# Optimization experiments

Measured on AMD Instinct MI355X. Metric: run time of the kernel, lower is better.

## Reference

```python
import jax, jax.numpy as jnp
import numpy as np
from jax.scipy.special import logsumexp

G, H, L, N, K = 2000, 128, 10, 4096, 10
TAU, LC, LA, EPS = 0.1, 1.0, 0.5, 1e-6

def _lin_init(k, fi, fo):
    return jax.random.normal(k, (fi, fo), jnp.float32) / np.sqrt(fi)

def setup_inputs():
    key = jax.random.key(0)
    ks = jax.random.split(key, 12)
    return {
        'wt_x': jax.random.normal(ks[0], (N, G), jnp.float32),
        'ko_x': jax.random.normal(ks[1], (N, G), jnp.float32),
        'wt_labels': jax.random.randint(ks[2], (N,), 0, K, dtype=jnp.int32),
        'ko_labels': jax.random.randint(ks[3], (N,), 0, K, dtype=jnp.int32),
        'enc_w1': _lin_init(ks[4], G, H), 'enc_b1': jnp.zeros((H,)),
        'enc_g': jnp.ones((H,)), 'enc_be': jnp.zeros((H,)),
        'enc_w2': _lin_init(ks[5], H, L), 'enc_b2': jnp.zeros((L,)),
        'kap_w1': _lin_init(ks[6], G, H), 'kap_b1': jnp.zeros((H,)),
        'kap_g': jnp.ones((H,)), 'kap_be': jnp.zeros((H,)),
        'kap_w2': _lin_init(ks[7], H, 1), 'kap_b2': jnp.zeros((1,)),
        'dec_w1': _lin_init(ks[8], L, H), 'dec_b1': jnp.zeros((H,)),
        'dec_g': jnp.ones((H,)), 'dec_be': jnp.zeros((H,)),
        'dec_w2': _lin_init(ks[9], H, G), 'dec_b2': jnp.zeros((G,)),
    }

def _mlp(x, w1, b1, g, be, w2, b2):
    # Linear -> LayerNorm -> ReLU -> Linear (dropout_prob=0)
    h = x @ w1 + b1
    m = h.mean(-1, keepdims=True)
    v = ((h - m) ** 2).mean(-1, keepdims=True)
    h = (h - m) / jnp.sqrt(v + 1e-5) * g + be
    return jax.nn.relu(h) @ w2 + b2

def _contrastive(z_wt, z_ko, y_wt, y_ko):
    S = (z_wt @ z_ko.T) / TAU  # [Nwt, Nko], unit-norm z so |S| <= 1/tau
    total = jnp.float32(0.0)
    n_shared = jnp.float32(0.0)
    for c in range(K):  # fixed small class count
        mwt = (y_wt == c).astype(S.dtype)
        mko = (y_ko == c).astype(S.dtype)
        n_wt, n_ko = mwt.sum(), mko.sum()
        valid = (n_wt > 0) & (n_ko > 0)
        nw, nk = jnp.maximum(n_wt, 1.0), jnp.maximum(n_ko, 1.0)
        # mean_{i in c, j in c} (LSE_i - S_ij) over ko columns of class c
        lse_r = logsumexp(jnp.where(mko[None, :] > 0, S, -1e4), axis=1)
        l1 = jnp.sum(mwt * (lse_r - (S @ mko) / nk)) / nw
        lse_c = logsumexp(jnp.where(mwt[:, None] > 0, S, -1e4), axis=0)
        l2 = jnp.sum(mko * (lse_c - (mwt @ S) / nw)) / nk
        total = total + jnp.where(valid, 0.5 * (l1 + l2), 0.0)
        n_shared = n_shared + valid.astype(S.dtype)
    return jnp.where(n_shared > 0, total / jnp.maximum(n_shared, 1.0), 0.0)

def _alignment(z, y):
    ones = jnp.ones(z.shape[0], z.dtype)
    counts = jax.ops.segment_sum(ones, y, num_segments=K)
    mu_c = jax.ops.segment_sum(z, y, num_segments=K) / jnp.maximum(counts, 1.0)[:, None]
    dev = z - mu_c[y]
    per_class = jax.ops.segment_sum(jnp.sum(dev ** 2, axis=1), y, num_segments=K) / jnp.maximum(counts, 1.0)
    present = counts > 0
    return jnp.sum(jnp.where(present, per_class, 0.0)) / jnp.maximum(jnp.sum(present.astype(z.dtype)), 1.0)

def reference(wt_x, ko_x, enc_w1, enc_b1, enc_g, enc_be, enc_w2, enc_b2, kap_w1, kap_b1, kap_g, kap_be, kap_w2, kap_b2, dec_w1, dec_b1, dec_g, dec_be, dec_w2, dec_b2, wt_labels, ko_labels):
    def encode(x):
        mu = _mlp(x, enc_w1, enc_b1, enc_g, enc_be, enc_w2, enc_b2)
        mu = mu / jnp.maximum(jnp.linalg.norm(mu, axis=1, keepdims=True), 1e-12)
        kappa = jax.nn.softplus(_mlp(x, kap_w1, kap_b1, kap_g, kap_be, kap_w2, kap_b2)) + EPS
        return mu, kappa
    wt_mu, wt_kappa = encode(wt_x)
    ko_mu, ko_kappa = encode(ko_x)
    wt_z, ko_z = wt_mu, ko_mu  # eval mode: z = mu (deterministic)
    wt_rec = _mlp(wt_z, dec_w1, dec_b1, dec_g, dec_be, dec_w2, dec_b2)
    ko_rec = _mlp(ko_z, dec_w1, dec_b1, dec_g, dec_be, dec_w2, dec_b2)
    recon = jnp.mean((wt_rec - wt_x) ** 2) + jnp.mean((ko_rec - ko_x) ** 2)
    kl = (wt_kappa.mean() + ko_kappa.mean()) * 0.01
    contrast = _contrastive(wt_z, ko_z, wt_labels, ko_labels)
    align = _alignment(jnp.concatenate([wt_z, ko_z], 0), jnp.concatenate([wt_labels, ko_labels], 0))
    return recon + kl + LC * contrast + LA * align
```

## Files before the change

kernel.cpp:

```cpp
#include <hip/hip_runtime.h>
#include <math.h>

typedef __attribute__((ext_vector_type(8))) __bf16 bf16x8;
typedef __attribute__((ext_vector_type(4))) float f32x4;

#define GL2LDS_(gptr, lptr) \
    __builtin_amdgcn_global_load_lds((const __attribute__((address_space(1))) void*)(gptr), \
                                     (__attribute__((address_space(3))) void*)(lptr), 16, 0, 0)

#define OFF_NWT   0
#define OFF_NKO   10
#define OFF_L1    20
#define OFF_L2    30
#define OFF_CNT   40
#define OFF_ZSUM  50
#define OFF_ZSQ   150
#define OFF_KSUM  160
#define OFF_REC   162
#define IOFF_WTOFF 192
#define IOFF_KOOFF 204
#define IOFF_WTCTR 216
#define IOFF_KOCTR 226
#define ACC_FLOATS 256

// ... 58 lines not shown
    for (int i = 0; i < 32; ++i) {
        int idx = i * 256 + t;
        int c = idx >> 6, jj = idx & 63;
        int j = j0 + jj;
        tile[jj][c] = (j < 2000) ? dw2[(size_t)c * 2000 + j] : 0.f;
    }
    __syncthreads();
#pragma unroll
    for (int i = 0; i < 32; ++i) {
        int idx = i * 256 + t;
        int jj = idx >> 7, c = idx & 127;
        float v = tile[jj][c];
        __bf16 h = (__bf16)v;
        size_t o = (size_t)(j0 + jj) * 128 + c;
        BThi[o] = h;
        BTlo[o] = (__bf16)(v - (float)h);
    }
}

__global__ void counts_kernel(const int* __restrict__ wtl, const int* __restrict__ kol,
                              float* __restrict__ acc)
{
    __shared__ int cw[10], ck[10];
    int t = threadIdx.x;
    if (t < 10) { cw[t] = 0; ck[t] = 0; }
    __syncthreads();
    for (int i = t; i < 4096; i += 1024) {
        atomicAdd(&cw[wtl[i]], 1);
        atomicAdd(&ck[kol[i]], 1);
    }
    __syncthreads();
    if (t < 10) { acc[OFF_NWT + t] = (float)cw[t]; acc[OFF_NKO + t] = (float)ck[t]; }
    if (t == 0) {
        int* ai = (int*)acc;
        int aw = 0, ak = 0;
        for (int c = 0; c < 10; ++c) {
            ai[IOFF_WTOFF + c] = aw; aw += cw[c];
            ai[IOFF_KOOFF + c] = ak; ak += ck[c];
        }
        ai[IOFF_WTOFF + 10] = aw;
        ai[IOFF_KOOFF + 10] = ak;
    }
}

__global__ __launch_bounds__(256) void scatter_z_kernel(const float* __restrict__ Z,
                                                        const int* __restrict__ wtl,
                                                        const int* __restrict__ kol,
                                                        float* __restrict__ acc,
                                                        float* __restrict__ ZcWT,
                                                        float* __restrict__ ZcKO)
{
    __shared__ int lcnt[20];
    __shared__ int lbase[20];
    int t = threadIdx.x;
    if (t < 20) lcnt[t] = 0;
    __syncthreads();
    int row = blockIdx.x * 256 + t;
    int side = row >= 4096;
    int r = side ? row - 4096 : row;
    int c = side ? kol[r] : wtl[r];
    int key = side * 10 + c;
    int myrank = atomicAdd(&lcnt[key], 1);
    __syncthreads();
    int* ai = (int*)acc;
    if (t < 20 && lcnt[t] > 0)
        lbase[t] = atomicAdd(&ai[IOFF_WTCTR + t], lcnt[t]);
    __syncthreads();
    int off = side ? ai[IOFF_KOOFF + c] : ai[IOFF_WTOFF + c];
    int slot = off + lbase[key] + myrank;
    float* dst = side ? ZcKO : ZcWT;
    const float* zr = Z + (size_t)row * 10;
#pragma unroll
    for (int d = 0; d < 10; ++d) dst[d * 4096 + slot] = zr[d];
}

__global__ __launch_bounds__(512) void gemm1_kernel(const float* __restrict__ wt_x,
                                                    const float* __restrict__ ko_x,
                                                    const __bf16* __restrict__ WThi,
                                                    const __bf16* __restrict__ WTlo,
                                                    float* __restrict__ Hb,
                                                    float* __restrict__ Hrest,
                                                    int nkc)
{
    __shared__ short Bs[2][2][4096];
    int t = threadIdx.x;
    int widx = t >> 6, lane = t & 63;
    int wm = widx >> 1, wn = widx & 1;
    int b = blockIdx.x;
    int mt = b & 63, strip = (b >> 6) & 1, kc = b >> 7;
    int R0 = mt * 128;
    int cb = strip * 128;
    int kchunk = 2048 / nkc;
    int kbase = kc * kchunk;
    int kleft = 2000 - kbase;
    int nsteps = (kleft < kchunk) ? ((kleft + 31) >> 5) : (kchunk >> 5);

    const float* xb = (R0 < 4096) ? (wt_x + (size_t)R0 * 2000)
                                  : (ko_x + (size_t)(R0 - 4096) * 2000);
    int ar = wm * 32 + (lane & 15);
    const float* xrow0 = xb + (size_t)ar * 2000 + kbase;
    const float* xrow1 = xrow0 + (size_t)16 * 2000;
    int kboff = (lane >> 4) * 8;

    int col0 = t >> 2;
    int s0   = (t & 3) ^ ((col0 >> 1) & 3);
    size_t boff = (size_t)(cb + col0) * 2048 + kbase + s0 * 8;
    const __bf16* bsrcH = WThi + boff;
    const __bf16* bsrcL = WTlo + boff;
    short* dstH0 = &Bs[0][0][t * 8];
    short* dstL0 = &Bs[0][1][t * 8];
    short* dstH1 = &Bs[1][0][t * 8];
    short* dstL1 = &Bs[1][1][t * 8];

    f32x4 acc00, acc01, acc02, acc03;
    f32x4 acc10, acc11, acc12, acc13;
#pragma unroll
    for (int r = 0; r < 4; ++r) {
        acc00[r]=0.f; acc01[r]=0.f; acc02[r]=0.f; acc03[r]=0.f;
        acc10[r]=0.f; acc11[r]=0.f; acc12[r]=0.f; acc13[r]=0.f;
    }

    float4 aA00, aA01, aA10, aA11;
    float4 aB00, aB01, aB10, aB11;

#define GLOADA_(step, a00, a01, a10, a11) do { \
    int k0_ = (step) * 32; \
    int k_ = k0_ + kboff; \
    if (kbase + k0_ <= 1952) { \
        a00 = *(const float4*)(xrow0 + k_); \
        a01 = *(const float4*)(xrow0 + k_ + 4); \
        a10 = *(const float4*)(xrow1 + k_); \
        a11 = *(const float4*)(xrow1 + k_ + 4); \
    } else { \
        float t0_[8], t1_[8]; \
        _Pragma("unroll") \
        for (int j = 0; j < 8; ++j) { \
            int kk = kbase + k_ + j; \
            t0_[j] = (kk < 2000) ? xrow0[k_ + j] : 0.f; \
            t1_[j] = (kk < 2000) ? xrow1[k_ + j] : 0.f; } \
        a00 = make_float4(t0_[0], t0_[1], t0_[2], t0_[3]); \
        a01 = make_float4(t0_[4], t0_[5], t0_[6], t0_[7]); \
        a10 = make_float4(t1_[0], t1_[1], t1_[2], t1_[3]); \
        a11 = make_float4(t1_[4], t1_[5], t1_[6], t1_[7]); } } while (0)

#define CONVA_(a0, a1, ahi, alo) do { \
    float av_[8] = {a0.x, a0.y, a0.z, a0.w, a1.x, a1.y, a1.z, a1.w}; \
    _Pragma("unroll") \
    for (int j = 0; j < 8; ++j) { \
        __bf16 h_ = (__bf16)av_[j]; \
        ahi[j] = h_; \
        alo[j] = (__bf16)(av_[j] - (float)h_); } } while (0)

#define MFMA_(buf, ahi0, alo0, ahi1, alo1) do { \
    _Pragma("unroll") \
    for (int nf = 0; nf < 4; ++nf) { \
        bf16x8 bhf = *(const bf16x8*)&Bs[buf][0][(ubase + nf * 64) * 8]; \
        bf16x8 blf = *(const bf16x8*)&Bs[buf][1][(ubase + nf * 64) * 8]; \
        f32x4* a0 = (nf == 0) ? &acc00 : (nf == 1) ? &acc01 : (nf == 2) ? &acc02 : &acc03; \
        f32x4* a1 = (nf == 0) ? &acc10 : (nf == 1) ? &acc11 : (nf == 2) ? &acc12 : &acc13; \
        *a0 = __builtin_amdgcn_mfma_f32_16x16x32_bf16(ahi0, bhf, *a0, 0, 0, 0); \
        *a0 = __builtin_amdgcn_mfma_f32_16x16x32_bf16(alo0, bhf, *a0, 0, 0, 0); \
        *a0 = __builtin_amdgcn_mfma_f32_16x16x32_bf16(ahi0, blf, *a0, 0, 0, 0); \
        *a1 = __builtin_amdgcn_mfma_f32_16x16x32_bf16(ahi1, bhf, *a1, 0, 0, 0); \
        *a1 = __builtin_amdgcn_mfma_f32_16x16x32_bf16(alo1, bhf, *a1, 0, 0, 0); \
        *a1 = __builtin_amdgcn_mfma_f32_16x16x32_bf16(ahi1, blf, *a1, 0, 0, 0); } } while (0)

    GL2LDS_(bsrcH, dstH0);
    GL2LDS_(bsrcL, dstL0);
    GLOADA_(0, aA00, aA01, aA10, aA11);
    if (1 < nsteps) GLOADA_(1, aB00, aB01, aB10, aB11);
    __syncthreads();

    int cpr = lane & 15;
    int pph = (lane >> 4) ^ ((cpr >> 1) & 3);
    int ubase = (wn * 64 + cpr) * 4 + pph;

    int niter = (nsteps + 1) >> 1;
    for (int it = 0; it < niter; ++it) {
        int st0 = it * 2;
        {
            if (st0 + 1 < nsteps) {
                GL2LDS_(bsrcH + (size_t)(st0 + 1) * 32, dstH1);
                GL2LDS_(bsrcL + (size_t)(st0 + 1) * 32, dstL1);
            }
            bf16x8 ahi0, alo0, ahi1, alo1;
            CONVA_(aA00, aA01, ahi0, alo0);
            CONVA_(aA10, aA11, ahi1, alo1);
            if (st0 + 2 < nsteps) GLOADA_(st0 + 2, aA00, aA01, aA10, aA11);
            MFMA_(0, ahi0, alo0, ahi1, alo1);
            __syncthreads();
        }
        if (st0 + 1 < nsteps) {
            if (st0 + 2 < nsteps) {
                GL2LDS_(bsrcH + (size_t)(st0 + 2) * 32, dstH0);
                GL2LDS_(bsrcL + (size_t)(st0 + 2) * 32, dstL0);
            }
            bf16x8 ahi0, alo0, ahi1, alo1;
            CONVA_(aB00, aB01, ahi0, alo0);
            CONVA_(aB10, aB11, ahi1, alo1);
            if (st0 + 3 < nsteps) GLOADA_(st0 + 3, aB00, aB01, aB10, aB11);
            MFMA_(1, ahi0, alo0, ahi1, alo1);
            __syncthreads();
        }
    }

    float* Hq = (kc == 0) ? Hb : (Hrest + (size_t)(kc - 1) * HPART);
#pragma unroll
    for (int r = 0; r < 4; ++r) {
        int row0 = R0 + wm * 32 + (lane >> 4) * 4 + r;
        size_t base0 = (size_t)row0 * 256 + cb + wn * 64 + (lane & 15);
        Hq[base0]      = acc00[r];
        Hq[base0 + 16] = acc01[r];
        Hq[base0 + 32] = acc02[r];
        Hq[base0 + 48] = acc03[r];
        size_t base1 = base0 + (size_t)16 * 256;
        Hq[base1]      = acc10[r];
        Hq[base1 + 16] = acc11[r];
        Hq[base1 + 32] = acc12[r];
        Hq[base1 + 48] = acc13[r];
    }
#undef GLOADA_
#undef CONVA_
#undef MFMA_
}

__global__ __launch_bounds__(128) void stage2_kernel(const float* __restrict__ Hb,
    const float* __restrict__ Hrest, int nkc,
    const float* __restrict__ enc_b1, const float* __restrict__ enc_g, const float* __restrict__ enc_be,
    const float* __restrict__ enc_w2, const float* __restrict__ enc_b2,
    const float* __restrict__ kap_b1, const float* __restrict__ kap_g, const float* __restrict__ kap_be,
    const float* __restrict__ kap_w2, const float* __restrict__ kap_b2,
    float* __restrict__ Z, float* __restrict__ Kap)
{
    __shared__ float sh[128];
    int row  = blockIdx.x;
    int wave = threadIdx.x >> 6;
    int lane = threadIdx.x & 63;
    size_t hoff = (size_t)row * 256 + wave * 128;
    const float* hb  = Hb + hoff;
    const float* b1 = wave ? kap_b1 : enc_b1;
    const float* gg = wave ? kap_g  : enc_g;
    const float* bb = wave ? kap_be : enc_be;

    float h0 = hb[lane]      + b1[lane];
    float h1 = hb[lane + 64] + b1[lane + 64];
    for (int j = 0; j + 1 < nkc; ++j) {
        const float* hr = Hrest + (size_t)j * HPART + hoff;
        h0 += hr[lane];
        h1 += hr[lane + 64];
    }
    float s = h0 + h1;
#pragma unroll
    for (int o = 32; o > 0; o >>= 1) s += __shfl_xor(s, o, 64);
    float m = s * (1.f / 128.f);
    float d0 = h0 - m, d1 = h1 - m;
    float v = d0 * d0 + d1 * d1;
#pragma unroll
    for (int o = 32; o > 0; o >>= 1) v += __shfl_xor(v, o, 64);
    v *= (1.f / 128.f);
    float sc = 1.f / sqrtf(v + 1e-5f);
    float r0 = fmaxf(fmaf(d0 * sc, gg[lane],      bb[lane]),      0.f);
    float r1 = fmaxf(fmaf(d1 * sc, gg[lane + 64], bb[lane + 64]), 0.f);

    if (wave == 0) { sh[lane] = r0; sh[lane + 64] = r1; }
    __syncthreads();

    if (wave == 0) {
        float mu = 0.f;
        if (lane < 10) {
            mu = enc_b2[lane];
            for (int c = 0; c < 128; ++c) mu = fmaf(sh[c], enc_w2[c * 10 + lane], mu);
        }
        float n2 = mu * mu;
#pragma unroll
        for (int o = 8; o > 0; o >>= 1) n2 += __shfl_xor(n2, o, 16);
        float inv = 1.f / fmaxf(sqrtf(n2), 1e-12f);
        if (lane < 10) Z[(size_t)row * 10 + lane] = mu * inv;
    } else {
        float p = r0 * kap_w2[lane] + r1 * kap_w2[lane + 64];
#pragma unroll
        for (int o = 32; o > 0; o >>= 1) p += __shfl_xor(p, o, 64);
        if (lane == 0) {
            float x = p + kap_b2[0];
            float sp = (x > 20.f) ? x : log1pf(expf(x));
            Kap[row] = sp + 1e-6f;
        }
    }
}

__global__ __launch_bounds__(256) void dec_act_kernel(const float* __restrict__ Zb,
    const float* __restrict__ dw1, const float* __restrict__ db1,
    const float* __restrict__ dg,  const float* __restrict__ dbe,
    __bf16* __restrict__ Ahi, __bf16* __restrict__ Alo)
{
    int wave = threadIdx.x >> 6;
    int lane = threadIdx.x & 63;
    int row = blockIdx.x * 4 + wave;
    const float* zr = Zb + (size_t)row * 10;
    float z[10];
#pragma unroll
    for (int d = 0; d < 10; ++d) z[d] = zr[d];
    int c0 = lane, c1 = lane + 64;
    float h0 = db1[c0], h1 = db1[c1];
#pragma unroll
    for (int d = 0; d < 10; ++d) {
        h0 = fmaf(z[d], dw1[d * 128 + c0], h0);
        h1 = fmaf(z[d], dw1[d * 128 + c1], h1);
    }
    float s = h0 + h1;
#pragma unroll
    for (int o = 32; o > 0; o >>= 1) s += __shfl_xor(s, o, 64);
    float m = s * (1.f / 128.f);
    float d0 = h0 - m, d1 = h1 - m;
    float v = d0 * d0 + d1 * d1;
#pragma unroll
    for (int o = 32; o > 0; o >>= 1) v += __shfl_xor(v, o, 64);
    v *= (1.f / 128.f);
    float sc = 1.f / sqrtf(v + 1e-5f);
    float a0 = fmaxf(fmaf(d0 * sc, dg[c0], dbe[c0]), 0.f);
    float a1 = fmaxf(fmaf(d1 * sc, dg[c1], dbe[c1]), 0.f);
    __bf16 h0b = (__bf16)a0, h1b = (__bf16)a1;
    size_t base = (size_t)row * 128;
    Ahi[base + c0] = h0b;                 Ahi[base + c1] = h1b;
    Alo[base + c0] = (__bf16)(a0 - (float)h0b);
    Alo[base + c1] = (__bf16)(a1 - (float)h1b);
}

__global__ __launch_bounds__(512, 4) void dec_gemm_kernel(
    const __bf16* __restrict__ Ahi, const __bf16* __restrict__ Alo,
    const __bf16* __restrict__ BThi, const __bf16* __restrict__ BTlo,
    const float* __restrict__ wt_x, const float* __restrict__ ko_x,
    const float* __restrict__ db2, float* __restrict__ acc)
{
    __shared__ short BsH[2][8192];
    __shared__ short BsL[2][8192];
    __shared__ float rs[8];
    int t = threadIdx.x;
    int widx = t >> 6, lane = t & 63;
    int wm = widx >> 2, wn = widx & 3;
    int R0 = (blockIdx.x >> 1) * 32;
    int T0 = (blockIdx.x & 1) * 16;
    const float* xbase = (R0 < 4096) ? wt_x : ko_x;
    int xr0 = ((R0 < 4096) ? R0 : R0 - 4096) + wm * 16 + (lane >> 4) * 4;

    size_t abase = (size_t)(R0 + wm * 16 + (lane & 15)) * 128 + (lane >> 4) * 8;
    bf16x8 ah0 = *(const bf16x8*)(Ahi + abase);
    bf16x8 ah1 = *(const bf16x8*)(Ahi + abase + 32);
    bf16x8 ah2 = *(const bf16x8*)(Ahi + abase + 64);
    bf16x8 ah3 = *(const bf16x8*)(Ahi + abase + 96);
    bf16x8 al0 = *(const bf16x8*)(Alo + abase);
    bf16x8 al1 = *(const bf16x8*)(Alo + abase + 32);
    bf16x8 al2 = *(const bf16x8*)(Alo + abase + 64);
    bf16x8 al3 = *(const bf16x8*)(Alo + abase + 96);

    int g0c = t >> 4,         g0s = t & 15;
    int g1c = (t + 512) >> 4, g1s = t & 15;
    int u0 = g0c * 16 + (g0s ^ (g0c & 7));
    int u1 = g1c * 16 + (g1s ^ (g1c & 7));

    int col_local = wn * 16 + (lane & 15);
    int cl7 = col_local & 7;
    int rb = col_local * 16;
    int sb = lane >> 4;

    uint4 hA0, hA1, lA0, lA1, hB0, hB1, lB0, lB1;

#define GLOADB_(tile, h0, h1, l0, l1) do { \
    size_t gb = (size_t)(tile) * 8192; \
    h0 = *(const uint4*)(BThi + gb + (size_t)t * 8); \
    h1 = *(const uint4*)(BThi + gb + (size_t)(t + 512) * 8); \
    l0 = *(const uint4*)(BTlo + gb + (size_t)t * 8); \
    l1 = *(const uint4*)(BTlo + gb + (size_t)(t + 512) * 8); } while (0)

#define DSWRITE_(buf, h0, h1, l0, l1) do { \
    *(uint4*)&BsH[buf][u0 * 8] = h0; \
    *(uint4*)&BsH[buf][u1 * 8] = h1; \
    *(uint4*)&BsL[buf][u0 * 8] = l0; \
    *(uint4*)&BsL[buf][u1 * 8] = l1; } while (0)

#define COMPUTE_(buf, tile) do { \
    int un0 = rb + ((sb +  0) ^ cl7); \
    int un1 = rb + ((sb +  4) ^ cl7); \
    int un2 = rb + ((sb +  8) ^ cl7); \
    int un3 = rb + ((sb + 12) ^ cl7); \
    bf16x8 bh0 = *(const bf16x8*)&BsH[buf][un0 * 8]; \
    bf16x8 bh1 = *(const bf16x8*)&BsH[buf][un1 * 8]; \
    bf16x8 bh2 = *(const bf16x8*)&BsH[buf][un2 * 8]; \
    bf16x8 bh3 = *(const bf16x8*)&BsH[buf][un3 * 8]; \
    bf16x8 bl0 = *(const bf16x8*)&BsL[buf][un0 * 8]; \
    bf16x8 bl1 = *(const bf16x8*)&BsL[buf][un1 * 8]; \
    bf16x8 bl2 = *(const bf16x8*)&BsL[buf][un2 * 8]; \
    bf16x8 bl3 = *(const bf16x8*)&BsL[buf][un3 * 8]; \
    f32x4 a4; \
    _Pragma("unroll") \
    for (int r = 0; r < 4; ++r) a4[r] = 0.f; \
    a4 = __builtin_amdgcn_mfma_f32_16x16x32_bf16(ah0, bh0, a4, 0, 0, 0); \
    a4 = __builtin_amdgcn_mfma_f32_16x16x32_bf16(al0, bh0, a4, 0, 0, 0); \
    a4 = __builtin_amdgcn_mfma_f32_16x16x32_bf16(ah0, bl0, a4, 0, 0, 0); \
    a4 = __builtin_amdgcn_mfma_f32_16x16x32_bf16(ah1, bh1, a4, 0, 0, 0); \
    a4 = __builtin_amdgcn_mfma_f32_16x16x32_bf16(al1, bh1, a4, 0, 0, 0); \
    a4 = __builtin_amdgcn_mfma_f32_16x16x32_bf16(ah1, bl1, a4, 0, 0, 0); \
    a4 = __builtin_amdgcn_mfma_f32_16x16x32_bf16(ah2, bh2, a4, 0, 0, 0); \
    a4 = __builtin_amdgcn_mfma_f32_16x16x32_bf16(al2, bh2, a4, 0, 0, 0); \
    a4 = __builtin_amdgcn_mfma_f32_16x16x32_bf16(ah2, bl2, a4, 0, 0, 0); \
    a4 = __builtin_amdgcn_mfma_f32_16x16x32_bf16(ah3, bh3, a4, 0, 0, 0); \
    a4 = __builtin_amdgcn_mfma_f32_16x16x32_bf16(al3, bh3, a4, 0, 0, 0); \
    a4 = __builtin_amdgcn_mfma_f32_16x16x32_bf16(ah3, bl3, a4, 0, 0, 0); \
    int col = (tile) * 64 + col_local; \
    if (col < 2000) { \
        float bb = db2[col]; \
        _Pragma("unroll") \
        for (int r = 0; r < 4; ++r) { \
            float xv = xbase[(size_t)(xr0 + r) * 2000 + col]; \
            float e = a4[r] + bb - xv; \
            rsum = fmaf(e, e, rsum); \
        } } } while (0)

    float rsum = 0.f;
    GLOADB_(T0 + 0, hA0, hA1, lA0, lA1);
    GLOADB_(T0 + 1, hB0, hB1, lB0, lB1);
    DSWRITE_(0, hA0, hA1, lA0, lA1);
    __syncthreads();

    for (int it = 0; it < 8; ++it) {
        int lt = it * 2;
        {
            if (lt + 2 < 16) GLOADB_(T0 + lt + 2, hA0, hA1, lA0, lA1);
            DSWRITE_(1, hB0, hB1, lB0, lB1);
            COMPUTE_(0, T0 + lt);
            __syncthreads();
        }
        {
            if (lt + 3 < 16) GLOADB_(T0 + lt + 3, hB0, hB1, lB0, lB1);
            if (lt + 2 < 16) DSWRITE_(0, hA0, hA1, lA0, lA1);
            COMPUTE_(1, T0 + lt + 1);
            __syncthreads();
        }
    }

#pragma unroll
    for (int o = 32; o > 0; o >>= 1) rsum += __shfl_xor(rsum, o, 64);
    if (lane == 0) rs[widx] = rsum;
    __syncthreads();
    if (t == 0) {
        float s = 0.f;
#pragma unroll
        for (int w = 0; w < 8; ++w) s += rs[w];
        atomicAdd(&acc[OFF_REC], s);
    }
#undef GLOADB_
#undef DSWRITE_
#undef COMPUTE_
}

#define MAXNB 768
__global__ __launch_bounds__(256) void contrast_kernel(const float* __restrict__ ZcWT,
                                                       const float* __restrict__ ZcKO,
                                                       float* __restrict__ acc)
{
    __shared__ float zb[MAXNB * 12];
    __shared__ float bsum[4];
    int b = blockIdx.x;
    int cs = b / 3, sub = b - cs * 3;
    int c = cs >> 1, side = cs & 1;
    const int* ai = (const int*)acc;
    int aStart = side ? ai[IOFF_KOOFF + c]     : ai[IOFF_WTOFF + c];
    int aEnd   = side ? ai[IOFF_KOOFF + c + 1] : ai[IOFF_WTOFF + c + 1];
    int bStart = side ? ai[IOFF_WTOFF + c]     : ai[IOFF_KOOFF + c];
    int bEnd   = side ? ai[IOFF_WTOFF + c + 1] : ai[IOFF_KOOFF + c + 1];
    int na = aEnd - aStart;
    int nb = bEnd - bStart;
    if (nb > MAXNB) nb = MAXNB;
    const float* ZA = side ? ZcKO : ZcWT;
    const float* ZB = side ? ZcWT : ZcKO;
    int t = threadIdx.x;

    for (int u = t; u < nb; u += 256) {
#pragma unroll
        for (int d = 0; d < 10; ++d) zb[u * 12 + d] = ZB[d * 4096 + bStart + u];
    }
    __syncthreads();

    int chunk = (na + 2) / 3;
    int r0 = sub * chunk;
    int rcnt = na - r0; if (rcnt > chunk) rcnt = chunk;

    float wsum = 0.f;
    bool waveActive = (nb > 0) && ((t & ~63) < rcnt);
    if (waveActive) {
        bool valid = t < rcnt;
        int ar = aStart + (valid ? (r0 + t) : 0);
        float za[10];
#pragma unroll
        for (int d = 0; d < 10; ++d) za[d] = ZA[d * 4096 + ar];
        float se = 0.f, ss = 0.f;
        for (int u = 0; u < nb; ++u) {
            const float* zp = &zb[u * 12];
            float s = 0.f;
#pragma unroll
            for (int d = 0; d < 10; ++d) s = fmaf(za[d], zp[d], s);
            s *= 10.f;
            se += __expf(s - 10.f);
            ss += s;
        }
        if (valid) wsum = (10.f + __logf(se)) - ss / (float)nb;
    }
#pragma unroll
    for (int o = 32; o > 0; o >>= 1) wsum += __shfl_xor(wsum, o, 64);
    if ((t & 63) == 0) bsum[t >> 6] = wsum;
    __syncthreads();
    if (t == 0) {
        float s = bsum[0] + bsum[1] + bsum[2] + bsum[3];
        if (s != 0.f || nb > 0)
            atomicAdd(&acc[(side ? OFF_L2 : OFF_L1) + c], s);
    }
}

__global__ __launch_bounds__(256) void align_kernel(const float* __restrict__ Z,
                                                    const int* __restrict__ wtl,
                                                    const int* __restrict__ kol,
                                                    const float* __restrict__ Kap,
                                                    float* __restrict__ Part)
{
    __shared__ float cL[10], qL[10], sL[100], ks;
    int t = threadIdx.x;
    if (t < 10) { cL[t] = 0.f; qL[t] = 0.f; }
    if (t < 100) sL[t] = 0.f;
    if (t == 0) ks = 0.f;
    __syncthreads();
    int row = blockIdx.x * 256 + t;
    int c = (row < 4096) ? wtl[row] : kol[row - 4096];
    float zz[10]; float q = 0.f;
#pragma unroll
    for (int d = 0; d < 10; ++d) { zz[d] = Z[(size_t)row * 10 + d]; q = fmaf(zz[d], zz[d], q); }
    atomicAdd(&cL[c], 1.f);
    atomicAdd(&qL[c], q);
#pragma unroll
    for (int d = 0; d < 10; ++d) atomicAdd(&sL[c * 10 + d], zz[d]);
    atomicAdd(&ks, Kap[row]);
    __syncthreads();
    float* pb = Part + (size_t)blockIdx.x * 128;
    if (t < 10)  { pb[t] = cL[t]; pb[10 + t] = qL[t]; }
    if (t < 100) pb[20 + t] = sL[t];
    if (t == 0)  pb[120] = ks;
}

__global__ void reduce_align_kernel(const float* __restrict__ Part, float* __restrict__ acc)
{
    int t = threadIdx.x;
    if (t < 120) {
        float s = 0.f;
        for (int b = 0; b < 32; ++b) s += Part[(size_t)b * 128 + t];
        if (t < 10)       acc[OFF_CNT + t] = s;
        else if (t < 20)  acc[OFF_ZSQ + t - 10] = s;
        else              acc[OFF_ZSUM + t - 20] = s;
    } else if (t == 120 || t == 121) {
        float s = 0.f;
        int b0 = (t - 120) * 16;
        for (int b = b0; b < b0 + 16; ++b) s += Part[(size_t)b * 128 + 120];
        acc[OFF_KSUM + (t - 120)] = s;
    }
}

__global__ void finalize_kernel(const float* __restrict__ acc, float* __restrict__ out)
{
    float total = 0.f, nsh = 0.f;
    for (int c = 0; c < 10; ++c) {
        float nw = acc[OFF_NWT + c], nk = acc[OFF_NKO + c];
        if (nw > 0.5f && nk > 0.5f) {
            float l1 = acc[OFF_L1 + c] / nw;
            float l2 = acc[OFF_L2 + c] / nk;
            total += 0.5f * (l1 + l2);
            nsh += 1.f;
        }
    }
    float contrast = (nsh > 0.f) ? total / nsh : 0.f;
    float ap = 0.f, np_ = 0.f;
    for (int c = 0; c < 10; ++c) {
        float cn = acc[OFF_CNT + c];
        if (cn > 0.5f) {
            float mu2 = 0.f;
            for (int d = 0; d < 10; ++d) {
                float mm = acc[OFF_ZSUM + c * 10 + d] / cn;
                mu2 = fmaf(mm, mm, mu2);
            }
            ap += acc[OFF_ZSQ + c] / cn - mu2;
            np_ += 1.f;
        }
    }
    float align = (np_ > 0.f) ? ap / np_ : 0.f;
    float kl = 0.01f * (acc[OFF_KSUM + 0] + acc[OFF_KSUM + 1]) * (1.f / 4096.f);
    float recon = acc[OFF_REC] * (1.f / 8192000.f);
    out[0] = recon + kl + 1.0f * contrast + 0.5f * align;
}

extern "C" void kernel_launch(void* const* d_in, const int* in_sizes, int n_in,
                              void* d_out, int out_size, void* d_ws, size_t ws_size,
                              hipStream_t stream)
{
    const float* wt_x   = (const float*)d_in[0];
    const float* ko_x   = (const float*)d_in[1];
    const int*   wtl    = (const int*)d_in[2];
    const int*   kol    = (const int*)d_in[3];
    const float* enc_w1 = (const float*)d_in[4];
    const float* enc_b1 = (const float*)d_in[5];
    const float* enc_g  = (const float*)d_in[6];
    const float* enc_be = (const float*)d_in[7];
    const float* enc_w2 = (const float*)d_in[8];
    const float* enc_b2 = (const float*)d_in[9];
    const float* kap_w1 = (const float*)d_in[10];
    const float* kap_b1 = (const float*)d_in[11];
    const float* kap_g  = (const float*)d_in[12];
    const float* kap_be = (const float*)d_in[13];
    const float* kap_w2 = (const float*)d_in[14];
    const float* kap_b2 = (const float*)d_in[15];
    const float* dw1    = (const float*)d_in[16];
    const float* db1    = (const float*)d_in[17];
    const float* dg     = (const float*)d_in[18];
    const float* dbe    = (const float*)d_in[19];
    const float* dw2    = (const float*)d_in[20];
    const float* db2    = (const float*)d_in[21];

    float* ws  = (float*)d_ws;
    float* acc = ws;
    __bf16* WThi = (__bf16*)(ws + WT_OFF);
    __bf16* WTlo = (__bf16*)(ws + WTLO_OFF);
    float* Hb    = ws + H_OFF;
    float* Zb    = ws + Z_OFF;
    float* Kap   = ws + KAP_OFF;
    float* Hrest = ws + HREST_OFF;
    __bf16* Ahi  = (__bf16*)(ws + ACT_HI_OFF);
    __bf16* Alo  = (__bf16*)(ws + ACT_LO_OFF);
    __bf16* BThi = (__bf16*)(ws + BT_HI_OFF);
    __bf16* BTlo = (__bf16*)(ws + BT_LO_OFF);
    float* ZcKO = ws + ZCKO_OFF;
    float* ZcWT = ws + ZCWT_OFF;
    float* Part = ws + PART_OFF;

    size_t need4 = (size_t)(HREST_OFF + 3 * HPART) * sizeof(float);
    int nkc = (ws_size >= need4) ? 4 : 2;

    hipMemsetAsync(acc, 0, ACC_FLOATS * sizeof(float), stream);
    pack_w_kernel<<<128, 256, 0, stream>>>(enc_w1, kap_w1, WThi, WTlo);
    counts_kernel<<<1, 1024, 0, stream>>>(wtl, kol, acc);
    gemm1_kernel<<<128 * nkc, 512, 0, stream>>>(wt_x, ko_x, WThi, WTlo, Hb, Hrest, nkc);
    stage2_kernel<<<8192, 128, 0, stream>>>(Hb, Hrest, nkc, enc_b1, enc_g, enc_be, enc_w2, enc_b2,
                                            kap_b1, kap_g, kap_be, kap_w2, kap_b2, Zb, Kap);
    pack_dw2_kernel<<<32, 256, 0, stream>>>(dw2, BThi, BTlo);
    dec_act_kernel<<<2048, 256, 0, stream>>>(Zb, dw1, db1, dg, dbe, Ahi, Alo);
    scatter_z_kernel<<<32, 256, 0, stream>>>(Zb, wtl, kol, acc, ZcWT, ZcKO);
    contrast_kernel<<<60, 256, 0, stream>>>(ZcWT, ZcKO, acc);
    align_kernel<<<32, 256, 0, stream>>>(Zb, wtl, kol, Kap, Part);
    reduce_align_kernel<<<1, 128, 0, stream>>>(Part, acc);
    dec_gemm_kernel<<<512, 512, 0, stream>>>(Ahi, Alo, BThi, BTlo, wt_x, ko_x, db2, acc);
    finalize_kernel<<<1, 1, 0, stream>>>(acc, (float*)d_out);
}
```

Baseline: 175.2 us.

## Double row tile in decoder GEMM, stage B via direct global-to-LDS loads, fuse align reduce

The decoder GEMM block now covers 64 rows and 8 column tiles instead of 32 rows and 16 tiles. This halves how often each block reloads the B operand per row and doubles the MFMA work per shared-memory B read. B staging moves from register-staged global loads plus ds_write to direct global_load_lds with the swizzle applied on the global address. The separate align reduction kernel is folded into a 128-thread finalize kernel to save one launch. The cost is more A registers per wave, which is why the launch bound's minimum blocks per CU drops from 4 to 2 and occupancy may fall.

```diff
diff --git a/kernel.cpp b/kernel.cpp
--- a/kernel.cpp
+++ b/kernel.cpp
@@ -408,7 +408,7 @@
     Alo[base + c1] = (__bf16)(a1 - (float)h1b);
 }
 
-__global__ __launch_bounds__(512, 4) void dec_gemm_kernel(
+__global__ __launch_bounds__(512, 2) void dec_gemm_kernel(
     const __bf16* __restrict__ Ahi, const __bf16* __restrict__ Alo,
     const __bf16* __restrict__ BThi, const __bf16* __restrict__ BTlo,
     const float* __restrict__ wt_x, const float* __restrict__ ko_x,
@@ -420,45 +420,47 @@
     int t = threadIdx.x;
     int widx = t >> 6, lane = t & 63;
     int wm = widx >> 2, wn = widx & 3;
-    int R0 = (blockIdx.x >> 1) * 32;
-    int T0 = (blockIdx.x & 1) * 16;
+    int R0 = (blockIdx.x >> 2) * 64;
+    int T0 = (blockIdx.x & 3) * 8;
     const float* xbase = (R0 < 4096) ? wt_x : ko_x;
-    int xr0 = ((R0 < 4096) ? R0 : R0 - 4096) + wm * 16 + (lane >> 4) * 4;
-
-    size_t abase = (size_t)(R0 + wm * 16 + (lane & 15)) * 128 + (lane >> 4) * 8;
-    bf16x8 ah0 = *(const bf16x8*)(Ahi + abase);
-    bf16x8 ah1 = *(const bf16x8*)(Ahi + abase + 32);
-    bf16x8 ah2 = *(const bf16x8*)(Ahi + abase + 64);
-    bf16x8 ah3 = *(const bf16x8*)(Ahi + abase + 96);
-    bf16x8 al0 = *(const bf16x8*)(Alo + abase);
-    bf16x8 al1 = *(const bf16x8*)(Alo + abase + 32);
-    bf16x8 al2 = *(const bf16x8*)(Alo + abase + 64);
-    bf16x8 al3 = *(const bf16x8*)(Alo + abase + 96);
-
-    int g0c = t >> 4,         g0s = t & 15;
-    int g1c = (t + 512) >> 4, g1s = t & 15;
-    int u0 = g0c * 16 + (g0s ^ (g0c & 7));
-    int u1 = g1c * 16 + (g1s ^ (g1c & 7));
+    int rloc = (R0 < 4096) ? R0 : R0 - 4096;
+    int xrA = rloc + wm * 16 + (lane >> 4) * 4;
+    int xrB = xrA + 32;
+
+    size_t abA = (size_t)(R0 + wm * 16 + (lane & 15)) * 128 + (lane >> 4) * 8;
+    size_t abB = abA + (size_t)32 * 128;
+    bf16x8 ah0 = *(const bf16x8*)(Ahi + abA);
+    bf16x8 ah1 = *(const bf16x8*)(Ahi + abA + 32);
+    bf16x8 ah2 = *(const bf16x8*)(Ahi + abA + 64);
+    bf16x8 ah3 = *(const bf16x8*)(Ahi + abA + 96);
+    bf16x8 ah4 = *(const bf16x8*)(Ahi + abB);
+    bf16x8 ah5 = *(const bf16x8*)(Ahi + abB + 32);
+    bf16x8 ah6 = *(const bf16x8*)(Ahi + abB + 64);
+    bf16x8 ah7 = *(const bf16x8*)(Ahi + abB + 96);
+    bf16x8 al0 = *(const bf16x8*)(Alo + abA);
+    bf16x8 al1 = *(const bf16x8*)(Alo + abA + 32);
+    bf16x8 al2 = *(const bf16x8*)(Alo + abA + 64);
+    bf16x8 al3 = *(const bf16x8*)(Alo + abA + 96);
+    bf16x8 al4 = *(const bf16x8*)(Alo + abB);
+    bf16x8 al5 = *(const bf16x8*)(Alo + abB + 32);
+    bf16x8 al6 = *(const bf16x8*)(Alo + abB + 64);
+    bf16x8 al7 = *(const bf16x8*)(Alo + abB + 96);
+
+    int u0 = t, u1 = t + 512;
+    size_t g0 = (size_t)((u0 >> 4) * 16 + ((u0 & 15) ^ ((u0 >> 4) & 7))) * 8;
+    size_t g1 = (size_t)((u1 >> 4) * 16 + ((u1 & 15) ^ ((u1 >> 4) & 7))) * 8;
+
+#define STAGE_(buf, tile) do { \
+    size_t gb = (size_t)(tile) * 8192; \
+    GL2LDS_(BThi + gb + g0, &BsH[buf][t * 8]); \
+    GL2LDS_(BThi + gb + g1, &BsH[buf][(t + 512) * 8]); \
+    GL2LDS_(BTlo + gb + g0, &BsL[buf][t * 8]); \
+    GL2LDS_(BTlo + gb + g1, &BsL[buf][(t + 512) * 8]); } while (0)
 
     int col_local = wn * 16 + (lane & 15);
     int cl7 = col_local & 7;
     int rb = col_local * 16;
     int sb = lane >> 4;
-
-    uint4 hA0, hA1, lA0, lA1, hB0, hB1, lB0, lB1;
-
-#define GLOADB_(tile, h0, h1, l0, l1) do { \
-    size_t gb = (size_t)(tile) * 8192; \
-    h0 = *(const uint4*)(BThi + gb + (size_t)t * 8); \
-    h1 = *(const uint4*)(BThi + gb + (size_t)(t + 512) * 8); \
-    l0 = *(const uint4*)(BTlo + gb + (size_t)t * 8); \
-    l1 = *(const uint4*)(BTlo + gb + (size_t)(t + 512) * 8); } while (0)
-
-#define DSWRITE_(buf, h0, h1, l0, l1) do { \
-    *(uint4*)&BsH[buf][u0 * 8] = h0; \
-    *(uint4*)&BsH[buf][u1 * 8] = h1; \
-    *(uint4*)&BsL[buf][u0 * 8] = l0; \
-    *(uint4*)&BsL[buf][u1 * 8] = l1; } while (0)
 
 #define COMPUTE_(buf, tile) do { \
     int un0 = rb + ((sb +  0) ^ cl7); \
@@ -473,49 +475,60 @@
     bf16x8 bl1 = *(const bf16x8*)&BsL[buf][un1 * 8]; \
     bf16x8 bl2 = *(const bf16x8*)&BsL[buf][un2 * 8]; \
     bf16x8 bl3 = *(const bf16x8*)&BsL[buf][un3 * 8]; \
-    f32x4 a4; \
+    f32x4 a4A, a4B; \
     _Pragma("unroll") \
-    for (int r = 0; r < 4; ++r) a4[r] = 0.f; \
-    a4 = __builtin_amdgcn_mfma_f32_16x16x32_bf16(ah0, bh0, a4, 0, 0, 0); \
-    a4 = __builtin_amdgcn_mfma_f32_16x16x32_bf16(al0, bh0, a4, 0, 0, 0); \
-    a4 = __builtin_amdgcn_mfma_f32_16x16x32_bf16(ah0, bl0, a4, 0, 0, 0); \
-    a4 = __builtin_amdgcn_mfma_f32_16x16x32_bf16(ah1, bh1, a4, 0, 0, 0); \
-    a4 = __builtin_amdgcn_mfma_f32_16x16x32_bf16(al1, bh1, a4, 0, 0, 0); \
-    a4 = __builtin_amdgcn_mfma_f32_16x16x32_bf16(ah1, bl1, a4, 0, 0, 0); \
-    a4 = __builtin_amdgcn_mfma_f32_16x16x32_bf16(ah2, bh2, a4, 0, 0, 0); \
-    a4 = __builtin_amdgcn_mfma_f32_16x16x32_bf16(al2, bh2, a4, 0, 0, 0); \
-    a4 = __builtin_amdgcn_mfma_f32_16x16x32_bf16(ah2, bl2, a4, 0, 0, 0); \
-    a4 = __builtin_amdgcn_mfma_f32_16x16x32_bf16(ah3, bh3, a4, 0, 0, 0); \
-    a4 = __builtin_amdgcn_mfma_f32_16x16x32_bf16(al3, bh3, a4, 0, 0, 0); \
-    a4 = __builtin_amdgcn_mfma_f32_16x16x32_bf16(ah3, bl3, a4, 0, 0, 0); \
+    for (int r = 0; r < 4; ++r) { a4A[r] = 0.f; a4B[r] = 0.f; } \
+    a4A = __builtin_amdgcn_mfma_f32_16x16x32_bf16(ah0, bh0, a4A, 0, 0, 0); \
+    a4A = __builtin_amdgcn_mfma_f32_16x16x32_bf16(al0, bh0, a4A, 0, 0, 0); \
+    a4A = __builtin_amdgcn_mfma_f32_16x16x32_bf16(ah0, bl0, a4A, 0, 0, 0); \
+    a4A = __builtin_amdgcn_mfma_f32_16x16x32_bf16(ah1, bh1, a4A, 0, 0, 0); \
+    a4A = __builtin_amdgcn_mfma_f32_16x16x32_bf16(al1, bh1, a4A, 0, 0, 0); \
+    a4A = __builtin_amdgcn_mfma_f32_16x16x32_bf16(ah1, bl1, a4A, 0, 0, 0); \
+    a4A = __builtin_amdgcn_mfma_f32_16x16x32_bf16(ah2, bh2, a4A, 0, 0, 0); \
+    a4A = __builtin_amdgcn_mfma_f32_16x16x32_bf16(al2, bh2, a4A, 0, 0, 0); \
+    a4A = __builtin_amdgcn_mfma_f32_16x16x32_bf16(ah2, bl2, a4A, 0, 0, 0); \
+    a4A = __builtin_amdgcn_mfma_f32_16x16x32_bf16(ah3, bh3, a4A, 0, 0, 0); \
+    a4A = __builtin_amdgcn_mfma_f32_16x16x32_bf16(al3, bh3, a4A, 0, 0, 0); \
+    a4A = __builtin_amdgcn_mfma_f32_16x16x32_bf16(ah3, bl3, a4A, 0, 0, 0); \
+    a4B = __builtin_amdgcn_mfma_f32_16x16x32_bf16(ah4, bh0, a4B, 0, 0, 0); \
+    a4B = __builtin_amdgcn_mfma_f32_16x16x32_bf16(al4, bh0, a4B, 0, 0, 0); \
+    a4B = __builtin_amdgcn_mfma_f32_16x16x32_bf16(ah4, bl0, a4B, 0, 0, 0); \
+    a4B = __builtin_amdgcn_mfma_f32_16x16x32_bf16(ah5, bh1, a4B, 0, 0, 0); \
+    a4B = __builtin_amdgcn_mfma_f32_16x16x32_bf16(al5, bh1, a4B, 0, 0, 0); \
+    a4B = __builtin_amdgcn_mfma_f32_16x16x32_bf16(ah5, bl1, a4B, 0, 0, 0); \
+    a4B = __builtin_amdgcn_mfma_f32_16x16x32_bf16(ah6, bh2, a4B, 0, 0, 0); \
+    a4B = __builtin_amdgcn_mfma_f32_16x16x32_bf16(al6, bh2, a4B, 0, 0, 0); \
+    a4B = __builtin_amdgcn_mfma_f32_16x16x32_bf16(ah6, bl2, a4B, 0, 0, 0); \
+    a4B = __builtin_amdgcn_mfma_f32_16x16x32_bf16(ah7, bh3, a4B, 0, 0, 0); \
+    a4B = __builtin_amdgcn_mfma_f32_16x16x32_bf16(al7, bh3, a4B, 0, 0, 0); \
+    a4B = __builtin_amdgcn_mfma_f32_16x16x32_bf16(ah7, bl3, a4B, 0, 0, 0); \
     int col = (tile) * 64 + col_local; \
     if (col < 2000) { \
         float bb = db2[col]; \
         _Pragma("unroll") \
         for (int r = 0; r < 4; ++r) { \
-            float xv = xbase[(size_t)(xr0 + r) * 2000 + col]; \
-            float e = a4[r] + bb - xv; \
-            rsum = fmaf(e, e, rsum); \
+            float xvA = xbase[(size_t)(xrA + r) * 2000 + col]; \
+            float eA = a4A[r] + bb - xvA; \
+            rsum = fmaf(eA, eA, rsum); \
+            float xvB = xbase[(size_t)(xrB + r) * 2000 + col]; \
+            float eB = a4B[r] + bb - xvB; \
+            rsum = fmaf(eB, eB, rsum); \
         } } } while (0)
 
     float rsum = 0.f;
-    GLOADB_(T0 + 0, hA0, hA1, lA0, lA1);
-    GLOADB_(T0 + 1, hB0, hB1, lB0, lB1);
-    DSWRITE_(0, hA0, hA1, lA0, lA1);
-    __syncthreads();
-
-    for (int it = 0; it < 8; ++it) {
-        int lt = it * 2;
+    STAGE_(0, T0);
+    __syncthreads();
+
+    for (int it = 0; it < 4; ++it) {
+        int lt = T0 + it * 2;
         {
-            if (lt + 2 < 16) GLOADB_(T0 + lt + 2, hA0, hA1, lA0, lA1);
-            DSWRITE_(1, hB0, hB1, lB0, lB1);
-            COMPUTE_(0, T0 + lt);
+            STAGE_(1, lt + 1);
+            COMPUTE_(0, lt);
             __syncthreads();
         }
         {
-            if (lt + 3 < 16) GLOADB_(T0 + lt + 3, hB0, hB1, lB0, lB1);
-            if (lt + 2 < 16) DSWRITE_(0, hA0, hA1, lA0, lA1);
-            COMPUTE_(1, T0 + lt + 1);
+            if (it < 3) STAGE_(0, lt + 2);
+            COMPUTE_(1, lt + 1);
             __syncthreads();
         }
     }
@@ -530,8 +543,7 @@
         for (int w = 0; w < 8; ++w) s += rs[w];
         atomicAdd(&acc[OFF_REC], s);
     }
-#undef GLOADB_
-#undef DSWRITE_
+#undef STAGE_
 #undef COMPUTE_
 }
 
@@ -627,53 +639,52 @@
     if (t == 0)  pb[120] = ks;
 }
 
-__global__ void reduce_align_kernel(const float* __restrict__ Part, float* __restrict__ acc)
-{
+__global__ void finalize_kernel(const float* __restrict__ Part,
+                                const float* __restrict__ acc,
+                                float* __restrict__ out)
+{
+    __shared__ float red[121];
     int t = threadIdx.x;
     if (t < 120) {
         float s = 0.f;
         for (int b = 0; b < 32; ++b) s += Part[(size_t)b * 128 + t];
-        if (t < 10)       acc[OFF_CNT + t] = s;
-        else if (t < 20)  acc[OFF_ZSQ + t - 10] = s;
-        else              acc[OFF_ZSUM + t - 20] = s;
-    } else if (t == 120 || t == 121) {
+        red[t] = s;
+    } else if (t == 120) {
         float s = 0.f;
-        int b0 = (t - 120) * 16;
-        for (int b = b0; b < b0 + 16; ++b) s += Part[(size_t)b * 128 + 120];
-        acc[OFF_KSUM + (t - 120)] = s;
-    }
-}
-
-__global__ void finalize_kernel(const float* __restrict__ acc, float* __restrict__ out)
-{
-    float total = 0.f, nsh = 0.f;
-    for (int c = 0; c < 10; ++c) {
-        float nw = acc[OFF_NWT + c], nk = acc[OFF_NKO + c];
-        if (nw > 0.5f && nk > 0.5f) {
-            float l1 = acc[OFF_L1 + c] / nw;
-            float l2 = acc[OFF_L2 + c] / nk;
-            total += 0.5f * (l1 + l2);
-            nsh += 1.f;
-        }
-    }
-    float contrast = (nsh > 0.f) ? total / nsh : 0.f;
-    float ap = 0.f, np_ = 0.f;
-    for (int c = 0; c < 10; ++c) {
-        float cn = acc[OFF_CNT + c];
-        if (cn > 0.5f) {
-            float mu2 = 0.f;
-            for (int d = 0; d < 10; ++d) {
-                float mm = acc[OFF_ZSUM + c * 10 + d] / cn;
-                mu2 = fmaf(mm, mm, mu2);
+        for (int b = 0; b < 32; ++b) s += Part[(size_t)b * 128 + 120];
+        red[120] = s;
+    }
+    __syncthreads();
+    if (t == 0) {
+        float total = 0.f, nsh = 0.f;
+        for (int c = 0; c < 10; ++c) {
+            float nw = acc[OFF_NWT + c], nk = acc[OFF_NKO + c];
+            if (nw > 0.5f && nk > 0.5f) {
+                float l1 = acc[OFF_L1 + c] / nw;
+                float l2 = acc[OFF_L2 + c] / nk;
+                total += 0.5f * (l1 + l2);
+                nsh += 1.f;
             }
-            ap += acc[OFF_ZSQ + c] / cn - mu2;
-            np_ += 1.f;
-        }
-    }
-    float align = (np_ > 0.f) ? ap / np_ : 0.f;
-    float kl = 0.01f * (acc[OFF_KSUM + 0] + acc[OFF_KSUM + 1]) * (1.f / 4096.f);
-    float recon = acc[OFF_REC] * (1.f / 8192000.f);
-    out[0] = recon + kl + 1.0f * contrast + 0.5f * align;
+        }
+        float contrast = (nsh > 0.f) ? total / nsh : 0.f;
+        float ap = 0.f, np_ = 0.f;
+        for (int c = 0; c < 10; ++c) {
+            float cn = red[c];
+            if (cn > 0.5f) {
+                float mu2 = 0.f;
+                for (int d = 0; d < 10; ++d) {
+                    float mm = red[20 + c * 10 + d] / cn;
+                    mu2 = fmaf(mm, mm, mu2);
+                }
+                ap += red[10 + c] / cn - mu2;
+                np_ += 1.f;
+            }
+        }
+        float align = (np_ > 0.f) ? ap / np_ : 0.f;
+        float kl = 0.01f * red[120] * (1.f / 4096.f);
+        float recon = acc[OFF_REC] * (1.f / 8192000.f);
+        out[0] = recon + kl + 1.0f * contrast + 0.5f * align;
+    }
 }
 
 extern "C" void kernel_launch(void* const* d_in, const int* in_sizes, int n_in,
@@ -733,7 +744,6 @@
     scatter_z_kernel<<<32, 256, 0, stream>>>(Zb, wtl, kol, acc, ZcWT, ZcKO);
     contrast_kernel<<<60, 256, 0, stream>>>(ZcWT, ZcKO, acc);
     align_kernel<<<32, 256, 0, stream>>>(Zb, wtl, kol, Kap, Part);
-    reduce_align_kernel<<<1, 128, 0, stream>>>(Part, acc);
     dec_gemm_kernel<<<512, 512, 0, stream>>>(Ahi, Alo, BThi, BTlo, wt_x, ko_x, db2, acc);
-    finalize_kernel<<<1, 1, 0, stream>>>(acc, (float*)d_out);
-}
+    finalize_kernel<<<1, 128, 0, stream>>>(Part, acc, (float*)d_out);
+}
```

Result: slower. 187.8 us (+7.2%).

## Double K-step per pipeline stage in gemm1 and fuse align reduction into finalize

Applied to the files above, without the earlier changes.

The gemm1 main loop now stages two 32-wide K slices of B per buffer and keeps two steps of A in registers per stage, so each barrier covers twice as much MFMA work and there are half as many __syncthreads. LDS use doubles and register pressure grows from the extra A prefetch registers. Separately, the reduce_align kernel is merged into finalize_kernel, which reduces the partial sums itself in shared memory, removing one kernel launch.

```diff
diff --git a/kernel.cpp b/kernel.cpp
--- a/kernel.cpp
+++ b/kernel.cpp
@@ -164,7 +164,7 @@
                                                     float* __restrict__ Hrest,
                                                     int nkc)
 {
-    __shared__ short Bs[2][2][4096];
+    __shared__ short Bs[2][2][2][4096];
     int t = threadIdx.x;
     int widx = t >> 6, lane = t & 63;
     int wm = widx >> 1, wn = widx & 1;
@@ -176,6 +176,7 @@
     int kbase = kc * kchunk;
     int kleft = 2000 - kbase;
     int nsteps = (kleft < kchunk) ? ((kleft + 31) >> 5) : (kchunk >> 5);
+    int ntiles = (nsteps + 1) >> 1;
 
     const float* xb = (R0 < 4096) ? (wt_x + (size_t)R0 * 2000)
                                   : (ko_x + (size_t)(R0 - 4096) * 2000);
@@ -189,10 +190,13 @@
     size_t boff = (size_t)(cb + col0) * 2048 + kbase + s0 * 8;
     const __bf16* bsrcH = WThi + boff;
     const __bf16* bsrcL = WTlo + boff;
-    short* dstH0 = &Bs[0][0][t * 8];
-    short* dstL0 = &Bs[0][1][t * 8];
-    short* dstH1 = &Bs[1][0][t * 8];
-    short* dstL1 = &Bs[1][1][t * 8];
+
+#define STAGEB_(buf, tl) do { \
+    int st_ = (tl) * 2; \
+    GL2LDS_(bsrcH + (size_t)st_ * 32,       &Bs[buf][0][0][t * 8]); \
+    GL2LDS_(bsrcH + (size_t)(st_ + 1) * 32, &Bs[buf][0][1][t * 8]); \
+    GL2LDS_(bsrcL + (size_t)st_ * 32,       &Bs[buf][1][0][t * 8]); \
+    GL2LDS_(bsrcL + (size_t)(st_ + 1) * 32, &Bs[buf][1][1][t * 8]); } while (0)
 
     f32x4 acc00, acc01, acc02, acc03;
     f32x4 acc10, acc11, acc12, acc13;
@@ -202,8 +206,8 @@
         acc10[r]=0.f; acc11[r]=0.f; acc12[r]=0.f; acc13[r]=0.f;
     }
 
-    float4 aA00, aA01, aA10, aA11;
-    float4 aB00, aB01, aB10, aB11;
+    float4 aA00, aA01, aA10, aA11, aA20, aA21, aA30, aA31;
+    float4 aB00, aB01, aB10, aB11, aB20, aB21, aB30, aB31;
 
 #define GLOADA_(step, a00, a01, a10, a11) do { \
     int k0_ = (step) * 32; \
@@ -233,11 +237,11 @@
         ahi[j] = h_; \
         alo[j] = (__bf16)(av_[j] - (float)h_); } } while (0)
 
-#define MFMA_(buf, ahi0, alo0, ahi1, alo1) do { \
+#define MFMAH_(buf, half, ahi0, alo0, ahi1, alo1) do { \
     _Pragma("unroll") \
     for (int nf = 0; nf < 4; ++nf) { \
-        bf16x8 bhf = *(const bf16x8*)&Bs[buf][0][(ubase + nf * 64) * 8]; \
-        bf16x8 blf = *(const bf16x8*)&Bs[buf][1][(ubase + nf * 64) * 8]; \
+        bf16x8 bhf = *(const bf16x8*)&Bs[buf][0][half][(ubase + nf * 64) * 8]; \
+        bf16x8 blf = *(const bf16x8*)&Bs[buf][1][half][(ubase + nf * 64) * 8]; \
         f32x4* a0 = (nf == 0) ? &acc00 : (nf == 1) ? &acc01 : (nf == 2) ? &acc02 : &acc03; \
         f32x4* a1 = (nf == 0) ? &acc10 : (nf == 1) ? &acc11 : (nf == 2) ? &acc12 : &acc13; \
         *a0 = __builtin_amdgcn_mfma_f32_16x16x32_bf16(ahi0, bhf, *a0, 0, 0, 0); \
@@ -247,41 +251,46 @@
         *a1 = __builtin_amdgcn_mfma_f32_16x16x32_bf16(alo1, bhf, *a1, 0, 0, 0); \
         *a1 = __builtin_amdgcn_mfma_f32_16x16x32_bf16(ahi1, blf, *a1, 0, 0, 0); } } while (0)
 
-    GL2LDS_(bsrcH, dstH0);
-    GL2LDS_(bsrcL, dstL0);
+    STAGEB_(0, 0);
     GLOADA_(0, aA00, aA01, aA10, aA11);
-    if (1 < nsteps) GLOADA_(1, aB00, aB01, aB10, aB11);
+    GLOADA_(1, aA20, aA21, aA30, aA31);
+    if (1 < ntiles) {
+        GLOADA_(2, aB00, aB01, aB10, aB11);
+        GLOADA_(3, aB20, aB21, aB30, aB31);
+    }
     __syncthreads();
 
     int cpr = lane & 15;
     int pph = (lane >> 4) ^ ((cpr >> 1) & 3);
     int ubase = (wn * 64 + cpr) * 4 + pph;
 
-    int niter = (nsteps + 1) >> 1;
-    for (int it = 0; it < niter; ++it) {
-        int st0 = it * 2;
+    int half_iters = (ntiles + 1) >> 1;
+    for (int it = 0; it < half_iters; ++it) {
+        int tl = it * 2;
         {
-            if (st0 + 1 < nsteps) {
-                GL2LDS_(bsrcH + (size_t)(st0 + 1) * 32, dstH1);
-                GL2LDS_(bsrcL + (size_t)(st0 + 1) * 32, dstL1);
+            if (tl + 1 < ntiles) STAGEB_(1, tl + 1);
+            bf16x8 h00,l00,h01,l01,h10,l10,h11,l11;
+            CONVA_(aA00, aA01, h00, l00); CONVA_(aA10, aA11, h01, l01);
+            CONVA_(aA20, aA21, h10, l10); CONVA_(aA30, aA31, h11, l11);
+            if (tl + 2 < ntiles) {
+                GLOADA_(2*(tl+2),   aA00, aA01, aA10, aA11);
+                GLOADA_(2*(tl+2)+1, aA20, aA21, aA30, aA31);
             }
-            bf16x8 ahi0, alo0, ahi1, alo1;
-            CONVA_(aA00, aA01, ahi0, alo0);
-            CONVA_(aA10, aA11, ahi1, alo1);
-            if (st0 + 2 < nsteps) GLOADA_(st0 + 2, aA00, aA01, aA10, aA11);
-            MFMA_(0, ahi0, alo0, ahi1, alo1);
+            MFMAH_(0, 0, h00, l00, h01, l01);
+            MFMAH_(0, 1, h10, l10, h11, l11);
             __syncthreads();
         }
-        if (st0 + 1 < nsteps) {
-            if (st0 + 2 < nsteps) {
-                GL2LDS_(bsrcH + (size_t)(st0 + 2) * 32, dstH0);
-                GL2LDS_(bsrcL + (size_t)(st0 + 2) * 32, dstL0);
+        if (tl + 1 < ntiles) {
+            if (tl + 2 < ntiles) STAGEB_(0, tl + 2);
+            bf16x8 h00,l00,h01,l01,h10,l10,h11,l11;
+            CONVA_(aB00, aB01, h00, l00); CONVA_(aB10, aB11, h01, l01);
+            CONVA_(aB20, aB21, h10, l10); CONVA_(aB30, aB31, h11, l11);
+            if (tl + 3 < ntiles) {
+                GLOADA_(2*(tl+3),   aB00, aB01, aB10, aB11);
+                GLOADA_(2*(tl+3)+1, aB20, aB21, aB30, aB31);
             }
-            bf16x8 ahi0, alo0, ahi1, alo1;
-            CONVA_(aB00, aB01, ahi0, alo0);
-            CONVA_(aB10, aB11, ahi1, alo1);
-            if (st0 + 3 < nsteps) GLOADA_(st0 + 3, aB00, aB01, aB10, aB11);
-            MFMA_(1, ahi0, alo0, ahi1, alo1);
+            MFMAH_(1, 0, h00, l00, h01, l01);
+            MFMAH_(1, 1, h10, l10, h11, l11);
             __syncthreads();
         }
     }
@@ -301,9 +310,10 @@
         Hq[base1 + 32] = acc12[r];
         Hq[base1 + 48] = acc13[r];
     }
+#undef STAGEB_
 #undef GLOADA_
 #undef CONVA_
-#undef MFMA_
+#undef MFMAH_
 }
 
 __global__ __launch_bounds__(128) void stage2_kernel(const float* __restrict__ Hb,
@@ -627,53 +637,52 @@
     if (t == 0)  pb[120] = ks;
 }
 
-__global__ void reduce_align_kernel(const float* __restrict__ Part, float* __restrict__ acc)
-{
+__global__ void finalize_kernel(const float* __restrict__ Part,
+                                const float* __restrict__ acc,
+                                float* __restrict__ out)
+{
+    __shared__ float red[121];
     int t = threadIdx.x;
     if (t < 120) {
         float s = 0.f;
         for (int b = 0; b < 32; ++b) s += Part[(size_t)b * 128 + t];
-        if (t < 10)       acc[OFF_CNT + t] = s;
-        else if (t < 20)  acc[OFF_ZSQ + t - 10] = s;
-        else              acc[OFF_ZSUM + t - 20] = s;
-    } else if (t == 120 || t == 121) {
+        red[t] = s;
+    } else if (t == 120) {
         float s = 0.f;
-        int b0 = (t - 120) * 16;
-        for (int b = b0; b < b0 + 16; ++b) s += Part[(size_t)b * 128 + 120];
-        acc[OFF_KSUM + (t - 120)] = s;
-    }
-}
-
-__global__ void finalize_kernel(const float* __restrict__ acc, float* __restrict__ out)
-{
-    float total = 0.f, nsh = 0.f;
-    for (int c = 0; c < 10; ++c) {
-        float nw = acc[OFF_NWT + c], nk = acc[OFF_NKO + c];
-        if (nw > 0.5f && nk > 0.5f) {
-            float l1 = acc[OFF_L1 + c] / nw;
-            float l2 = acc[OFF_L2 + c] / nk;
-            total += 0.5f * (l1 + l2);
-            nsh += 1.f;
-        }
-    }
-    float contrast = (nsh > 0.f) ? total / nsh : 0.f;
-    float ap = 0.f, np_ = 0.f;
-    for (int c = 0; c < 10; ++c) {
-        float cn = acc[OFF_CNT + c];
-        if (cn > 0.5f) {
-            float mu2 = 0.f;
-            for (int d = 0; d < 10; ++d) {
-                float mm = acc[OFF_ZSUM + c * 10 + d] / cn;
-                mu2 = fmaf(mm, mm, mu2);
+        for (int b = 0; b < 32; ++b) s += Part[(size_t)b * 128 + 120];
+        red[120] = s;
+    }
+    __syncthreads();
+    if (t == 0) {
+        float total = 0.f, nsh = 0.f;
+        for (int c = 0; c < 10; ++c) {
+            float nw = acc[OFF_NWT + c], nk = acc[OFF_NKO + c];
+            if (nw > 0.5f && nk > 0.5f) {
+                float l1 = acc[OFF_L1 + c] / nw;
+                float l2 = acc[OFF_L2 + c] / nk;
+                total += 0.5f * (l1 + l2);
+                nsh += 1.f;
             }
-            ap += acc[OFF_ZSQ + c] / cn - mu2;
-            np_ += 1.f;
-        }
-    }
-    float align = (np_ > 0.f) ? ap / np_ : 0.f;
-    float kl = 0.01f * (acc[OFF_KSUM + 0] + acc[OFF_KSUM + 1]) * (1.f / 4096.f);
-    float recon = acc[OFF_REC] * (1.f / 8192000.f);
-    out[0] = recon + kl + 1.0f * contrast + 0.5f * align;
+        }
+        float contrast = (nsh > 0.f) ? total / nsh : 0.f;
+        float ap = 0.f, np_ = 0.f;
+        for (int c = 0; c < 10; ++c) {
+            float cn = red[c];
+            if (cn > 0.5f) {
+                float mu2 = 0.f;
+                for (int d = 0; d < 10; ++d) {
+                    float mm = red[20 + c * 10 + d] / cn;
+                    mu2 = fmaf(mm, mm, mu2);
+                }
+                ap += red[10 + c] / cn - mu2;
+                np_ += 1.f;
+            }
+        }
+        float align = (np_ > 0.f) ? ap / np_ : 0.f;
+        float kl = 0.01f * red[120] * (1.f / 4096.f);
+        float recon = acc[OFF_REC] * (1.f / 8192000.f);
+        out[0] = recon + kl + 1.0f * contrast + 0.5f * align;
+    }
 }
 
 extern "C" void kernel_launch(void* const* d_in, const int* in_sizes, int n_in,
@@ -733,7 +742,6 @@
     scatter_z_kernel<<<32, 256, 0, stream>>>(Zb, wtl, kol, acc, ZcWT, ZcKO);
     contrast_kernel<<<60, 256, 0, stream>>>(ZcWT, ZcKO, acc);
     align_kernel<<<32, 256, 0, stream>>>(Zb, wtl, kol, Kap, Part);
-    reduce_align_kernel<<<1, 128, 0, stream>>>(Part, acc);
     dec_gemm_kernel<<<512, 512, 0, stream>>>(Ahi, Alo, BThi, BTlo, wt_x, ko_x, db2, acc);
-    finalize_kernel<<<1, 1, 0, stream>>>(acc, (float*)d_out);
-}
+    finalize_kernel<<<1, 128, 0, stream>>>(Part, acc, (float*)d_out);
+}
```

Result: no change. 174.5 us (-0.4%).
